# Performance work log

Hardware: AMD Instinct MI355X
Metric: run time of the kernel (lower is better)

## Reference

```python
import jax, jax.numpy as jnp
import numpy as np

NUM_HEADS = 8


def _mab(Q, K, Wq, bq, Wk, bk, Wv, bv, Wo, bo):
    # MAB with ln=False, dropout=0 (eval). Scale is sqrt(dim_V), matching source.
    B, Lq, _ = Q.shape
    Lk = K.shape[1]
    Dv = Wq.shape[1]
    dh = Dv // NUM_HEADS
    q = (Q @ Wq + bq).reshape(B, Lq, NUM_HEADS, dh).transpose(0, 2, 1, 3)
    k = (K @ Wk + bk).reshape(B, Lk, NUM_HEADS, dh).transpose(0, 2, 1, 3)
    v = (K @ Wv + bv).reshape(B, Lk, NUM_HEADS, dh).transpose(0, 2, 1, 3)
    A = jax.nn.softmax(jnp.einsum('bhqd,bhkd->bhqk', q, k) / jnp.sqrt(jnp.float32(Dv)), axis=-1)
    O = (q + jnp.einsum('bhqk,bhkd->bhqd', A, v)).transpose(0, 2, 1, 3).reshape(B, Lq, Dv)
    return O + jax.nn.relu(O @ Wo + bo)


def _forward(x, adj, gin_W, gin_b, geW1, geb1, geW2, geb2,
             gnW1, gnb1, gnW2, gnb2, goW, gob, S,
             mWq, mbq, mWk, mbk, mWv, mbv, mWo, mbo, finW, finb):
    B, V, T, D = x.shape
    Hd = gin_W.shape[1]
    # --- GNN encoder (adj path) ---
    h = x.reshape(B, V, T * D) @ gin_W + gin_b            # [B,V,H]
    # edge_mlp first linear on cat([h_i,h_j]) == h@Wi (row) + h@Wj (col); avoids 2H concat
    Wi, Wj = geW1[:Hd], geW1[Hd:]
    pre = (h @ Wi)[:, :, None, :] + (h @ Wj)[:, None, :, :] + geb1   # [B,V,V,H]
    e = jax.nn.relu(jax.nn.relu(pre) @ geW2 + geb2)       # [B,V,V,H]
    agg = jnp.einsum('bijh,bij->bih', e, adj)             # mask * sum over j, fused
    node = jax.nn.relu(jax.nn.relu(agg @ gnW1 + gnb1) @ gnW2 + gnb2)
    enc = node @ goW + gob                                # [B,V,H]
    # --- decoder: PMA + SAB + SAB + Linear ---
    o = _mab(jnp.broadcast_to(S, (B,) + S.shape[1:]), enc,
             mWq[0], mbq[0], mWk[0], mbk[0], mWv[0], mbv[0], mWo[0], mbo[0])
    o = _mab(o, o, mWq[1], mbq[1], mWk[1], mbk[1], mWv[1], mbv[1], mWo[1], mbo[1])
    o = _mab(o, o, mWq[2], mbq[2], mWk[2], mbk[2], mWv[2], mbv[2], mWo[2], mbo[2])
    out = o @ finW + finb                                 # [B,num_slots,T*OD]
    return out.reshape(B, S.shape[1], T, finW.shape[1] // T)


def setup_inputs() -> dict:
    key = jax.random.key(0)
    ks = jax.random.split(key, 16)
    B, V, T, D = 4, 256, 12, 4
    H, NS, OD = 256, 16, 32

    def w(k, shape, s=0.02):
        return s * jax.random.normal(k, shape, jnp.float32)

    return {
        'x': jax.random.normal(ks[0], (B, V, T, D), jnp.float32),
        'adj': (jax.random.uniform(ks[1], (B, V, V)) > 0.5).astype(jnp.float32),
        'gin_W': w(ks[2], (T * D, H)), 'gin_b': jnp.zeros((H,), jnp.float32),
        'geW1': w(ks[3], (2 * H, H)), 'geb1': jnp.zeros((H,), jnp.float32),
        'geW2': w(ks[4], (H, H)), 'geb2': jnp.zeros((H,), jnp.float32),
        'gnW1': w(ks[5], (H, H)), 'gnb1': jnp.zeros((H,), jnp.float32),
        'gnW2': w(ks[6], (H, H)), 'gnb2': jnp.zeros((H,), jnp.float32),
        'goW': w(ks[7], (H, H)), 'gob': jnp.zeros((H,), jnp.float32),
        'S': w(ks[8], (1, NS, H), 0.05),
        'mWq': w(ks[9], (3, H, H)), 'mbq': jnp.zeros((3, H), jnp.float32),
        'mWk': w(ks[10], (3, H, H)), 'mbk': jnp.zeros((3, H), jnp.float32),
        'mWv': w(ks[11], (3, H, H)), 'mbv': jnp.zeros((3, H), jnp.float32),
        'mWo': w(ks[12], (3, H, H)), 'mbo': jnp.zeros((3, H), jnp.float32),
        'finW': w(ks[13], (H, T * OD)), 'finb': jnp.zeros((T * OD,), jnp.float32),
    }


def reference(x, adj, gin_W, gin_b, geW1, geb1, geW2, geb2,
              gnW1, gnb1, gnW2, gnb2, goW, gob, S,
              mWq, mbq, mWk, mbk, mWv, mbv, mWo, mbo, finW, finb):
    return _forward(x, adj, gin_W, gin_b, geW1, geb1, geW2, geb2,
                    gnW1, gnb1, gnW2, gnb2, goW, gob, S,
                    mWq, mbq, mWk, mbk, mWv, mbv, mWo, mbo, finW, finb)
```

## Files before the change

kernel.cpp:

```cpp
#include <hip/hip_runtime.h>
#include <hip/hip_bf16.h>

typedef unsigned short u16;
typedef __bf16 bf8v __attribute__((ext_vector_type(8)));
typedef float f4v __attribute__((ext_vector_type(4)));

__device__ __forceinline__ float b2f(u16 v) {
  union { unsigned u; float f; } x; x.u = ((unsigned)v) << 16; return x.f;
}
__device__ __forceinline__ u16 f2b(float f) {
  union { float f; unsigned u; } x; x.f = f;
  unsigned r = (x.u + 0x7FFFu + ((x.u >> 16) & 1u)) >> 16;
  return (u16)r;
}
__device__ __forceinline__ unsigned pkbf(float a, float b) {
  union { __hip_bfloat162 h; unsigned u; } c;
  c.h = __float22bfloat162_rn(make_float2(a, b));
  return c.u;
}
__device__ __forceinline__ void up2(unsigned u, float& lo, float& hi) {
  union { unsigned x; float f; } a, b;
  a.x = u << 16; b.x = u & 0xffff0000u; lo = a.f; hi = b.f;
}

#define NFRAG 16
struct HeadArgs {
  const float* fsrc[NFRAG];
  u16* fdst[NFRAG];
  int fstride[NFRAG];
  int fbase[NFRAG + 1];
  int fragTiles, prepBid, q1Bid;
  const float *x, *ginW, *ginb, *geW1;
  float* hWiF;
  u16* hWjB;
  const float *mbk, *mbv, *mbq, *S, *mWq;
  float *bkv0, *bqkv1, *bqkv2;
  u16* q1b;
};

__global__ __launch_bounds__(256) void k_head(HeadArgs a) {
  __shared__ __align__(16) char sm[46080];
  const int bid = blockIdx.x, t = threadIdx.x;

  if (bid < 64) {
    u16* As = (u16*)sm;
    float* xs = (float*)(sm + 33792);
    const int lane = t & 63, wv = t >> 6;
    const int m0 = (bid >> 2) * 64, n0 = (bid & 3) * 128;
    for (int idx = t; idx < 64 * 48; idx += 256)
      xs[idx] = a.x[(size_t)(m0 + idx / 48) * 48 + idx % 48];
    __syncthreads();
    {
      float w48[48];
#pragma unroll
      for (int k = 0; k < 48; k++) w48[k] = a.ginW[(size_t)k * 256 + t];
      const float bias = a.ginb[t];
      for (int rg = 0; rg < 16; rg++) {
        float acc[4] = {bias, bias, bias, bias};
#pragma unroll
        for (int k = 0; k < 48; k++) {
          const float w = w48[k];
#pragma unroll
          for (int r = 0; r < 4; r++) acc[r] += xs[(rg * 4 + r) * 48 + k] * w;
        }
#pragma unroll
        for (int r = 0; r < 4; r++) As[(rg * 4 + r) * 264 + t] = f2b(acc[r]);
      }
    }
    __syncthreads();
    f4v acc[4][2];
// ... 48 lines not shown
  const int pb = bid - 64;
  if (pb < a.fragTiles) {
    u16* ld = (u16*)sm;
    int j = 0;
    while (j + 1 < NFRAG && a.fbase[j + 1] <= pb) j++;
    const int localT = pb - a.fbase[j];
    const float* src = a.fsrc[j];
    const int Ns = a.fstride[j];
    const int n0 = localT * 16;
    {
      const float* s = src + (size_t)t * Ns + n0;
      const float4 v0 = ((const float4*)s)[0], v1 = ((const float4*)s)[1];
      const float4 v2 = ((const float4*)s)[2], v3 = ((const float4*)s)[3];
      unsigned* row = (unsigned*)(ld + t * 20);
      row[0] = pkbf(v0.x, v0.y); row[1] = pkbf(v0.z, v0.w);
      row[2] = pkbf(v1.x, v1.y); row[3] = pkbf(v1.z, v1.w);
      row[4] = pkbf(v2.x, v2.y); row[5] = pkbf(v2.z, v2.w);
      row[6] = pkbf(v3.x, v3.y); row[7] = pkbf(v3.z, v3.w);
    }
    __syncthreads();
    u16* dst = a.fdst[j] + (size_t)localT * 4096;
#pragma unroll
    for (int s2 = 0; s2 < 2; s2++) {
      const int o = t * 2 + s2, kt = o >> 6, lane = o & 63;
      const int nlo = lane & 15, bk = kt * 32 + ((lane >> 4) << 3);
      union { u16 h[8]; uint4 q; } pk;
#pragma unroll
      for (int j2 = 0; j2 < 8; j2++) pk.h[j2] = ld[(bk + j2) * 20 + nlo];
      *(uint4*)(dst + (size_t)(kt * 64 + lane) * 8) = pk.q;
    }
    return;
  }
  if (bid == a.prepBid) {
    a.bkv0[t] = a.mbk[t]; a.bkv0[256 + t] = a.mbv[t];
    a.bqkv1[t] = a.mbq[256 + t]; a.bqkv1[256 + t] = a.mbk[256 + t]; a.bqkv1[512 + t] = a.mbv[256 + t];
    a.bqkv2[t] = a.mbq[512 + t]; a.bqkv2[256 + t] = a.mbk[512 + t]; a.bqkv2[512 + t] = a.mbv[512 + t];
    return;
  }
  if (bid == a.q1Bid) {
    float* Ss = (float*)sm;
    for (int idx = t; idx < 4096; idx += 256) Ss[idx] = a.S[idx];
    __syncthreads();
    float acc[16];
#pragma unroll
    for (int r = 0; r < 16; r++) acc[r] = 0.f;
    for (int k = 0; k < 256; k++) {
      const float w = a.mWq[(size_t)k * 256 + t];
#pragma unroll
      for (int r = 0; r < 16; r++) acc[r] += Ss[r * 256 + k] * w;
    }
    const float bq = a.mbq[t];
#pragma unroll
    for (int r = 0; r < 16; r++) a.q1b[r * 256 + t] = f2b(acc[r] + bq);
    return;
  }
}

__global__ __launch_bounds__(256) void k_edge(
    const float* __restrict__ hWiF, const u16* __restrict__ hWjB,
    const float* __restrict__ adj, const float* __restrict__ geb1,
    const u16* __restrict__ fragW2, const float* __restrict__ geb2,
    u16* __restrict__ aggB) {
  __shared__ __align__(16) u16 As[64 * 280];
  __shared__ float hi[256];
  __shared__ int jlist[256];
  __shared__ int cnt;
  const int t = threadIdx.x, lane = t & 63, wv = t >> 6;
  const int b = blockIdx.x >> 8, i = blockIdx.x & 255;
  if (t == 0) cnt = 0;
  __syncthreads();
  {
    const float a = adj[(size_t)(b * 256 + i) * 256 + t];
    hi[t] = hWiF[(size_t)(b * 256 + i) * 256 + t] + geb1[t];
    if (a != 0.f) { const int p = atomicAdd(&cnt, 1); jlist[p] = t; }
  }
  __syncthreads();
  const int nact = cnt;
  if (nact == 0) {
    if (lane < 16) {
#pragma unroll
      for (int nt = 0; nt < 4; nt++)
        aggB[(size_t)(b * 256 + i) * 256 + wv * 64 + nt * 16 + lane] = 0;
    }
    return;
  }
  const int nch = (nact + 63) >> 6;
  float bias2[4];
#pragma unroll
  for (int nt = 0; nt < 4; nt++) bias2[nt] = geb2[wv * 64 + nt * 16 + (lane & 15)];
  float aggAcc[4] = {0.f, 0.f, 0.f, 0.f};
  const u16* fw = fragW2 + lane * 8;
  const int r = t >> 2, q = t & 3;

  uint4 G[8];
  {
    const int rows0 = min(64, nact);
    const int j = (r < rows0) ? jlist[r] : jlist[0];
    const uint4* s4 = (const uint4*)(hWjB + (size_t)(b * 256 + j) * 256 + q * 64);
#pragma unroll
    for (int ii = 0; ii < 8; ii++) G[ii] = s4[ii];
  }

  for (int c = 0; c < nch; c++) {
    const int rows = min(64, nact - c * 64);
    {
      u16* dstrow = As + r * 280 + q * 72;
#pragma unroll
      for (int ii = 0; ii < 8; ii++) {
        const uint4 v = G[ii];
        const int k = q * 64 + ii * 8;
        float f0, f1, f2, f3, f4, f5, f6, f7;
        up2(v.x, f0, f1); up2(v.y, f2, f3); up2(v.z, f4, f5); up2(v.w, f6, f7);
        uint4 qd;
        qd.x = pkbf(fmaxf(f0 + hi[k + 0], 0.f), fmaxf(f1 + hi[k + 1], 0.f));
        qd.y = pkbf(fmaxf(f2 + hi[k + 2], 0.f), fmaxf(f3 + hi[k + 3], 0.f));
        qd.z = pkbf(fmaxf(f4 + hi[k + 4], 0.f), fmaxf(f5 + hi[k + 5], 0.f));
        qd.w = pkbf(fmaxf(f6 + hi[k + 6], 0.f), fmaxf(f7 + hi[k + 7], 0.f));
        *(uint4*)(dstrow + ii * 8) = qd;
      }
    }
    __syncthreads();
    if (c + 1 < nch) {
      const int rowsN = min(64, nact - (c + 1) * 64);
      const int j = (r < rowsN) ? jlist[(c + 1) * 64 + r] : jlist[0];
      const uint4* s4 = (const uint4*)(hWjB + (size_t)(b * 256 + j) * 256 + q * 64);
#pragma unroll
      for (int ii = 0; ii < 8; ii++) G[ii] = s4[ii];
    }
    f4v acc[4][4];
#pragma unroll
    for (int jt = 0; jt < 4; jt++)
#pragma unroll
      for (int nt = 0; nt < 4; nt++) acc[jt][nt] = (f4v){0.f, 0.f, 0.f, 0.f};
#pragma unroll
    for (int kt = 0; kt < 8; kt++) {
      bf8v af[4];
      const int coff = (kt >> 1) * 72 + (kt & 1) * 32 + ((lane >> 4) << 3);
#pragma unroll
      for (int jt = 0; jt < 4; jt++)
        af[jt] = *(const bf8v*)(As + (jt * 16 + (lane & 15)) * 280 + coff);
#pragma unroll
      for (int nt = 0; nt < 4; nt++) {
        const bf8v bw = *(const bf8v*)(fw + (size_t)((wv * 4 + nt) * 8 + kt) * 512);
#pragma unroll
        for (int jt = 0; jt < 4; jt++)
          acc[jt][nt] = __builtin_amdgcn_mfma_f32_16x16x32_bf16(af[jt], bw, acc[jt][nt], 0, 0, 0);
      }
    }
    const int rbase = (lane >> 4) * 4;
#pragma unroll
    for (int nt = 0; nt < 4; nt++) {
      float s = 0.f;
#pragma unroll
      for (int jt = 0; jt < 4; jt++) {
        const int r0 = jt * 16 + rbase;
#pragma unroll
        for (int rr = 0; rr < 4; rr++) {
          const float e = fmaxf(acc[jt][nt][rr] + bias2[nt], 0.f);
          s += (r0 + rr < rows) ? e : 0.f;
        }
      }
      s += __shfl_xor(s, 16);
      s += __shfl_xor(s, 32);
      aggAcc[nt] += s;
    }
    __syncthreads();
  }
  if (lane < 16) {
#pragma unroll
    for (int nt = 0; nt < 4; nt++) {
      const int n = wv * 64 + nt * 16 + lane;
      aggB[(size_t)(b * 256 + i) * 256 + n] = f2b(aggAcc[nt]);
    }
  }
}

#define NBLK 32

__device__ __forceinline__ void gridbar(int* cnt, int gen) {
  __syncthreads();
  if (threadIdx.x == 0) {
    __threadfence();
    __hip_atomic_fetch_add(cnt, 1, __ATOMIC_RELAXED, __HIP_MEMORY_SCOPE_AGENT);
    int it = 0;
    while (__hip_atomic_load(cnt, __ATOMIC_RELAXED, __HIP_MEMORY_SCOPE_AGENT) < NBLK * gen) {
      __builtin_amdgcn_s_sleep(8);
      if (((++it) & 255) == 0)
        __hip_atomic_fetch_add(cnt, 0, __ATOMIC_RELAXED, __HIP_MEMORY_SCOPE_AGENT);
    }
    __threadfence();
  }
  __syncthreads();
}

__device__ void g32(const u16* Al, const u16* frag, const float* bias, int relu,
                    u16* Ol, int t) {
  const int lane = t & 63, wv = t >> 6;
  f4v acc[2][4];
#pragma unroll
  for (int mt = 0; mt < 2; mt++)
#pragma unroll
    for (int nt = 0; nt < 4; nt++) acc[mt][nt] = (f4v){0.f, 0.f, 0.f, 0.f};
#pragma unroll
  for (int kt = 0; kt < 8; kt++) {
    bf8v af[2], bf[4];
#pragma unroll
    for (int mt = 0; mt < 2; mt++)
      af[mt] = *(const bf8v*)(Al + (mt * 16 + (lane & 15)) * 264 + kt * 32 + ((lane >> 4) << 3));
#pragma unroll
    for (int nt = 0; nt < 4; nt++)
      bf[nt] = *(const bf8v*)(frag + ((size_t)((wv * 4 + nt) * 8 + kt) * 64 + lane) * 8);
#pragma unroll
    for (int mt = 0; mt < 2; mt++)
#pragma unroll
      for (int nt = 0; nt < 4; nt++)
        acc[mt][nt] = __builtin_amdgcn_mfma_f32_16x16x32_bf16(af[mt], bf[nt], acc[mt][nt], 0, 0, 0);
  }
#pragma unroll
  for (int mt = 0; mt < 2; mt++)
#pragma unroll
    for (int nt = 0; nt < 4; nt++) {
      const int col = wv * 64 + nt * 16 + (lane & 15);
      const float bv = bias[col];
#pragma unroll
      for (int r = 0; r < 4; r++) {
        const int row = mt * 16 + ((lane >> 4) << 2) + r;
        float v = acc[mt][nt][r] + bv;
        if (relu) v = fmaxf(v, 0.f);
        Ol[row * 264 + col] = f2b(v);
      }
    }
}

__device__ void g32kv(const u16* Al, const u16* frag, const float* bias,
                      u16* outG, int t) {
  const int lane = t & 63, wv = t >> 6;
  f4v acc[2][8];
#pragma unroll
  for (int mt = 0; mt < 2; mt++)
#pragma unroll
    for (int nt = 0; nt < 8; nt++) acc[mt][nt] = (f4v){0.f, 0.f, 0.f, 0.f};
#pragma unroll
  for (int kt = 0; kt < 8; kt++) {
    bf8v af[2];
#pragma unroll
    for (int mt = 0; mt < 2; mt++)
      af[mt] = *(const bf8v*)(Al + (mt * 16 + (lane & 15)) * 264 + kt * 32 + ((lane >> 4) << 3));
#pragma unroll
    for (int nt = 0; nt < 8; nt++) {
      const bf8v bf = *(const bf8v*)(frag + ((size_t)((wv * 8 + nt) * 8 + kt) * 64 + lane) * 8);
#pragma unroll
      for (int mt = 0; mt < 2; mt++)
        acc[mt][nt] = __builtin_amdgcn_mfma_f32_16x16x32_bf16(af[mt], bf, acc[mt][nt], 0, 0, 0);
    }
  }
#pragma unroll
  for (int mt = 0; mt < 2; mt++)
#pragma unroll
    for (int nt = 0; nt < 8; nt++) {
      const int col = wv * 128 + nt * 16 + (lane & 15);
      const float bv = bias[col];
#pragma unroll
      for (int r = 0; r < 4; r++) {
        const int row = mt * 16 + ((lane >> 4) << 2) + r;
        outG[(size_t)row * 512 + col] = f2b(acc[mt][nt][r] + bv);
      }
    }
}

__device__ void attn_tile(const u16* __restrict__ qbuf,
                          const u16* __restrict__ kbuf, const u16* __restrict__ vbuf,
                          float* __restrict__ oF, u16* __restrict__ oB,
                          int b, int hd, float* qs, float* sc, float* vs, int t) {
  const int lane = t & 63, wv = t >> 6;
  const int Lk = 256;
  if (t < 64) {
    const int row = t >> 2, part = t & 3;
    const uint4 q4 = *(const uint4*)(qbuf + (size_t)row * 256 + hd * 32 + part * 8);
    float f0, f1, f2, f3, f4, f5, f6, f7;
    up2(q4.x, f0, f1); up2(q4.y, f2, f3); up2(q4.z, f4, f5); up2(q4.w, f6, f7);
    float4* d = (float4*)(qs + row * 32 + part * 8);
    d[0] = make_float4(f0, f1, f2, f3);
    d[1] = make_float4(f4, f5, f6, f7);
  }
  __syncthreads();
  {
    float kv[32];
    const uint4* kp = (const uint4*)(kbuf + (size_t)(b * Lk + t) * 512 + hd * 32);
#pragma unroll
    for (int c4 = 0; c4 < 4; c4++) {
      const uint4 k4 = kp[c4];
      up2(k4.x, kv[c4 * 8 + 0], kv[c4 * 8 + 1]);
      up2(k4.y, kv[c4 * 8 + 2], kv[c4 * 8 + 3]);
      up2(k4.z, kv[c4 * 8 + 4], kv[c4 * 8 + 5]);
      up2(k4.w, kv[c4 * 8 + 6], kv[c4 * 8 + 7]);
    }
    for (int r = 0; r < 16; r++) {
      float s = 0.f;
#pragma unroll
      for (int d = 0; d < 32; d++) s += qs[r * 32 + d] * kv[d];
      sc[r * 256 + t] = s * 0.0625f;
    }
  }
  __syncthreads();
  for (int r = wv * 4; r < wv * 4 + 4; r++) {
    float v[4];
    float mx = -1e30f;
#pragma unroll
    for (int q2 = 0; q2 < 4; q2++) {
      v[q2] = sc[r * 256 + lane + q2 * 64];
      mx = fmaxf(mx, v[q2]);
    }
    for (int off = 32; off; off >>= 1) mx = fmaxf(mx, __shfl_xor(mx, off));
    float sum = 0.f;
#pragma unroll
    for (int q2 = 0; q2 < 4; q2++) { v[q2] = __expf(v[q2] - mx); sum += v[q2]; }
    for (int off = 32; off; off >>= 1) sum += __shfl_xor(sum, off);
    const float inv = 1.f / sum;
#pragma unroll
    for (int q2 = 0; q2 < 4; q2++) sc[r * 256 + lane + q2 * 64] = v[q2] * inv;
  }
  __syncthreads();
  for (int u = t; u < 1024; u += 256) {
    const int row = u >> 2, part = u & 3;
    const uint4 v4 = *(const uint4*)(vbuf + (size_t)(b * Lk + row) * 512 + hd * 32 + part * 8);
    float f0, f1, f2, f3, f4, f5, f6, f7;
    up2(v4.x, f0, f1); up2(v4.y, f2, f3); up2(v4.z, f4, f5); up2(v4.w, f6, f7);
    float4* d = (float4*)(vs + row * 32 + part * 8);
    d[0] = make_float4(f0, f1, f2, f3);
    d[1] = make_float4(f4, f5, f6, f7);
  }
  __syncthreads();
  const int r0 = t >> 5, d = t & 31;
  float a0 = qs[r0 * 32 + d], a1 = qs[(r0 + 8) * 32 + d];
#pragma unroll 4
  for (int j = 0; j < Lk; j++) {
    const float vv = vs[j * 32 + d];
    a0 += sc[r0 * 256 + j] * vv;
    a1 += sc[(r0 + 8) * 256 + j] * vv;
  }
  const int c0 = hd * 32 + d;
  oF[(size_t)(b * 16 + r0) * 256 + c0] = a0;
  oB[(size_t)(b * 16 + r0) * 256 + c0] = f2b(a0);
  oF[(size_t)(b * 16 + r0 + 8) * 256 + c0] = a1;
  oB[(size_t)(b * 16 + r0 + 8) * 256 + c0] = f2b(a1);
}

__device__ void wprojG(const u16* __restrict__ o1b, const float* __restrict__ o1f,
                       const u16* __restrict__ frag, const float* __restrict__ bias,
                       u16* actL, float* residL, int b, int T, int lane) {
  f4v acc = (f4v){0.f, 0.f, 0.f, 0.f};
  const u16* abase = o1b + (size_t)(b * 16 + (lane & 15)) * 256 + ((lane >> 4) << 3);
  const u16* fbase = frag + ((size_t)(T * 8) * 64 + lane) * 8;
#pragma unroll
  for (int kt = 0; kt < 8; kt++)
    acc = __builtin_amdgcn_mfma_f32_16x16x32_bf16(*(const bf8v*)(abase + kt * 32),
                                                  *(const bf8v*)(fbase + (size_t)kt * 512), acc, 0, 0, 0);
  const int col = T * 16 + (lane & 15);
  const float bv = bias[col];
#pragma unroll
  for (int r = 0; r < 4; r++) {
    const int row = ((lane >> 4) << 2) + r;
    const float v = fmaxf(acc[r] + bv, 0.f) + o1f[(size_t)(b * 16 + row) * 256 + col];
    residL[row * 256 + col] = v;
    actL[row * 264 + col] = f2b(v);
  }
}

__device__ void wprojQ(const u16* actL, const u16* __restrict__ frag,
                       const float* __restrict__ bias, u16* qkvL, int T, int lane) {
  f4v acc = (f4v){0.f, 0.f, 0.f, 0.f};
  const u16* abase = actL + (lane & 15) * 264 + ((lane >> 4) << 3);
  const u16* fbase = frag + ((size_t)(T * 8) * 64 + lane) * 8;
#pragma unroll
  for (int kt = 0; kt < 8; kt++)
    acc = __builtin_amdgcn_mfma_f32_16x16x32_bf16(*(const bf8v*)(abase + kt * 32),
                                                  *(const bf8v*)(fbase + (size_t)kt * 512), acc, 0, 0, 0);
  const int col = T * 16 + (lane & 15);
// ... 79 lines not shown
  }
  float mx = fmaxf(fmaxf(p[0], p[1]), fmaxf(p[2], p[3]));
  mx = fmaxf(mx, __shfl_xor(mx, 16));
  mx = fmaxf(mx, __shfl_xor(mx, 32));
  float sum = 0.f;
#pragma unroll
  for (int c = 0; c < 4; c++) { p[c] = __expf(p[c] - mx); sum += p[c]; }
  sum += __shfl_xor(sum, 16);
  sum += __shfl_xor(sum, 32);
  const float inv = 1.f / sum;
#pragma unroll
  for (int c = 0; c < 4; c++) ps[r * 16 + cg * 4 + c] = p[c] * inv;
  float o[8];
#pragma unroll
  for (int j = 0; j < 8; j++) o[j] = qv[cg * 8 + j];
#pragma unroll
  for (int c = 0; c < 16; c++) {
    const float pv = ps[r * 16 + c];
    const uint4 v4 = *(const uint4*)(qkvL + c * 776 + 512 + hd * 32 + cg * 8);
    float v0, v1;
    up2(v4.x, v0, v1); o[0] += pv * v0; o[1] += pv * v1;
    up2(v4.y, v0, v1); o[2] += pv * v0; o[3] += pv * v1;
    up2(v4.z, v0, v1); o[4] += pv * v0; o[5] += pv * v1;
    up2(v4.w, v0, v1); o[6] += pv * v0; o[7] += pv * v1;
  }
  const int col0 = hd * 32 + cg * 8;
#pragma unroll
  for (int j = 0; j < 8; j++) residL[r * 256 + col0 + j] = o[j];
  unsigned* ob = (unsigned*)(actOut + r * 264 + col0);
  ob[0] = pkbf(o[0], o[1]); ob[1] = pkbf(o[2], o[3]);
  ob[2] = pkbf(o[4], o[5]); ob[3] = pkbf(o[6], o[7]);
}

struct TailArgs {
  const u16 *agg, *fGn1, *fGn2, *fGo, *fKV0, *fQKV1, *fQKV2, *fO0, *fO1, *fO2, *fFin, *q1b;
  const float *gnb1, *gnb2, *gob, *bkv0, *bqkv1, *bqkv2, *mbo, *finb;
  u16 *kv1, *o1b;
  float *o1f, *outF;
  int* bar;
};

__global__ __launch_bounds__(256) void k_tail(TailArgs a) {
  __shared__ __align__(16) char smem[62208];
  const int bid = blockIdx.x, t = threadIdx.x;
  const int lane = t & 63, w = t >> 6;

  {
    u16* actA = (u16*)smem;
    u16* actB = (u16*)(smem + 16896);
    const int r0 = bid * 32;
#pragma unroll
    for (int s = 0; s < 4; s++) {
      const int u = t * 4 + s, row = u >> 5, ch = u & 31;
      *(uint4*)(actA + row * 264 + ch * 8) =
          *(const uint4*)(a.agg + (size_t)(r0 + row) * 256 + ch * 8);
    }
    __syncthreads();
    g32(actA, a.fGn1, a.gnb1, 1, actB, t); __syncthreads();
    g32(actB, a.fGn2, a.gnb2, 1, actA, t); __syncthreads();
    g32(actA, a.fGo, a.gob, 0, actB, t); __syncthreads();
    g32kv(actB, a.fKV0, a.bkv0, a.kv1 + (size_t)r0 * 512, t);
  }
  gridbar(a.bar, 1);
  {
    float* qs = (float*)smem;
    float* sc = (float*)(smem + 2048);
    float* vs = (float*)(smem + 18432);
    attn_tile(a.q1b, a.kv1, a.kv1 + 256, a.o1f, a.o1b, bid >> 3, bid & 7, qs, sc, vs, t);
  }
  gridbar(a.bar, 2);
  if (bid >= 4) return;
  {
    const int b = bid;
    u16* act0 = (u16*)smem;
    u16* act1 = (u16*)(smem + 8448);
    u16* qkvL = (u16*)(smem + 16896);
    float* residL = (float*)(smem + 41728);
    float* psL = (float*)(smem + 58112);
    __syncthreads();
    for (int T = w; T < 16; T += 4) wprojG(a.o1b, a.o1f, a.fO0, a.mbo, act0, residL, b, T, lane);
    __syncthreads();
    for (int T = w; T < 48; T += 4) wprojQ(act0, a.fQKV1, a.bqkv1, qkvL, T, lane);
    __syncthreads();
    for (int hd = w; hd < 8; hd += 4) attnB(qkvL, residL, act1, psL + w * 256, hd, lane);
    __syncthreads();
    for (int T = w; T < 16; T += 4) wprojR(act1, a.fO1, a.mbo + 256, act0, residL, T, lane);
    __syncthreads();
    for (int T = w; T < 48; T += 4) wprojQ(act0, a.fQKV2, a.bqkv2, qkvL, T, lane);
    __syncthreads();
    for (int hd = w; hd < 8; hd += 4) attnB(qkvL, residL, act1, psL + w * 256, hd, lane);
    __syncthreads();
    for (int T = w; T < 16; T += 4) wprojR(act1, a.fO2, a.mbo + 512, act0, residL, T, lane);
    __syncthreads();
    for (int T = w; T < 24; T += 4)
      wprojF(act0, a.fFin, a.finb, a.outF + (size_t)b * 16 * 384, T, lane);
  }
}

extern "C" void kernel_launch(void* const* d_in, const int* in_sizes, int n_in,
                              void* d_out, int out_size, void* d_ws, size_t ws_size,
                              hipStream_t stream) {
  const float* x    = (const float*)d_in[0];
  const float* adj  = (const float*)d_in[1];
  const float* ginW = (const float*)d_in[2];
  const float* ginb = (const float*)d_in[3];
  const float* geW1 = (const float*)d_in[4];
  const float* geb1 = (const float*)d_in[5];
  const float* geW2 = (const float*)d_in[6];
  const float* geb2 = (const float*)d_in[7];
  const float* gnW1 = (const float*)d_in[8];
  const float* gnb1 = (const float*)d_in[9];
  const float* gnW2 = (const float*)d_in[10];
  const float* gnb2 = (const float*)d_in[11];
  const float* goW  = (const float*)d_in[12];
  const float* gob  = (const float*)d_in[13];
  const float* S    = (const float*)d_in[14];
  const float* mWq  = (const float*)d_in[15];
  const float* mbq  = (const float*)d_in[16];
  const float* mWk  = (const float*)d_in[17];
  const float* mbk  = (const float*)d_in[18];
  const float* mWv  = (const float*)d_in[19];
  const float* mbv  = (const float*)d_in[20];
  const float* mWo  = (const float*)d_in[21];
  const float* mbo  = (const float*)d_in[22];
  const float* finW = (const float*)d_in[23];
  const float* finb = (const float*)d_in[24];
  (void)in_sizes; (void)n_in; (void)out_size; (void)ws_size;

  char* wp = (char*)d_ws;
// ... 26 lines not shown
  u16* o1b      = (u16*)alloc(64 * 256 * 2);
  int* bar      = (int*)alloc(256);

  HeadArgs H{};
  int nj = 0, tiles = 0;
  auto addF = [&](const float* s, int stride, u16* d, int nT) {
    H.fsrc[nj] = s; H.fdst[nj] = d; H.fstride[nj] = stride; H.fbase[nj] = tiles;
    tiles += nT; nj++;
  };
  addF(geW2, 256, fW2, 16);
  addF(gnW1, 256, fGn1, 16);
  addF(gnW2, 256, fGn2, 16);
  addF(goW, 256, fGo, 16);
  addF(mWk, 256, fKV0, 16);
  addF(mWv, 256, fKV0 + 16 * 4096, 16);
  addF(mWq + 65536, 256, fQKV1, 16);
  addF(mWk + 65536, 256, fQKV1 + 16 * 4096, 16);
  addF(mWv + 65536, 256, fQKV1 + 32 * 4096, 16);
  addF(mWq + 131072, 256, fQKV2, 16);
  addF(mWk + 131072, 256, fQKV2 + 16 * 4096, 16);
  addF(mWv + 131072, 256, fQKV2 + 32 * 4096, 16);
  addF(mWo, 256, fO0, 16);
  addF(mWo + 65536, 256, fO1, 16);
  addF(mWo + 131072, 256, fO2, 16);
  addF(finW, 384, fFin, 24);
  H.fbase[nj] = tiles;
  H.fragTiles = tiles;
  H.prepBid = 64 + tiles;
  H.q1Bid = 64 + tiles + 1;
  H.x = x; H.ginW = ginW; H.ginb = ginb; H.geW1 = geW1;
  H.hWiF = hWiF; H.hWjB = hWjB;
  H.mbk = mbk; H.mbv = mbv; H.mbq = mbq; H.S = S; H.mWq = mWq;
  H.bkv0 = bkv0; H.bqkv1 = bqkv1; H.bqkv2 = bqkv2; H.q1b = q1b;

  TailArgs T{};
  T.agg = agg_b; T.fGn1 = fGn1; T.fGn2 = fGn2; T.fGo = fGo; T.fKV0 = fKV0;
  T.fQKV1 = fQKV1; T.fQKV2 = fQKV2; T.fO0 = fO0; T.fO1 = fO1; T.fO2 = fO2;
  T.fFin = fFin; T.q1b = q1b;
  T.gnb1 = gnb1; T.gnb2 = gnb2; T.gob = gob;
  T.bkv0 = bkv0; T.bqkv1 = bqkv1; T.bqkv2 = bqkv2; T.mbo = mbo; T.finb = finb;
  T.kv1 = kv1; T.o1b = o1b; T.o1f = o1f; T.outF = (float*)d_out;
  T.bar = bar;

  hipMemsetAsync(bar, 0, 256, stream);
  k_head<<<dim3(64 + tiles + 2), dim3(256), 0, stream>>>(H);
  k_edge<<<dim3(1024), dim3(256), 0, stream>>>(hWiF, hWjB, adj, geb1, fW2, geb2, agg_b);
  k_tail<<<dim3(NBLK), dim3(256), 0, stream>>>(T);
}
```

Baseline: 259.7 us.

## Fuse edge kernel with node MLP and attention via counter barrier; split tail

Merges the edge aggregation kernel with the node MLP, KV projection and PMA attention stages into one 1024-block kernel. All blocks increment a global counter and the first 32 blocks spin on it before continuing, replacing a kernel boundary and the memset with an in-kernel reset done in the head kernel. The final SAB stages move to a separate 4-block kernel, and the KV projection is split into halves to cut register use. It relies on the first 32 blocks making progress while the other blocks finish, and it adds spin-wait costs on those 32 blocks.

```diff
diff --git a/kernel.cpp b/kernel.cpp
--- a/kernel.cpp
+++ b/kernel.cpp
@@ -36,6 +36,7 @@
   const float *mbk, *mbv, *mbq, *S, *mWq;
   float *bkv0, *bqkv1, *bqkv2;
   u16* q1b;
+  int* bar;
 };
 
 __global__ __launch_bounds__(256) void k_head(HeadArgs a) {
@@ -150,6 +151,7 @@
     return;
   }
   if (bid == a.prepBid) {
+    if (t < 8) a.bar[t] = 0;
     a.bkv0[t] = a.mbk[t]; a.bkv0[256 + t] = a.mbv[t];
     a.bqkv1[t] = a.mbq[256 + t]; a.bqkv1[256 + t] = a.mbk[256 + t]; a.bqkv1[512 + t] = a.mbv[256 + t];
     a.bqkv2[t] = a.mbq[512 + t]; a.bqkv2[256 + t] = a.mbk[512 + t]; a.bqkv2[512 + t] = a.mbv[512 + t];
@@ -172,143 +174,6 @@
     for (int r = 0; r < 16; r++) a.q1b[r * 256 + t] = f2b(acc[r] + bq);
     return;
   }
-}
-
-__global__ __launch_bounds__(256) void k_edge(
-    const float* __restrict__ hWiF, const u16* __restrict__ hWjB,
-    const float* __restrict__ adj, const float* __restrict__ geb1,
-    const u16* __restrict__ fragW2, const float* __restrict__ geb2,
-    u16* __restrict__ aggB) {
-  __shared__ __align__(16) u16 As[64 * 280];
-  __shared__ float hi[256];
-  __shared__ int jlist[256];
-  __shared__ int cnt;
-  const int t = threadIdx.x, lane = t & 63, wv = t >> 6;
-  const int b = blockIdx.x >> 8, i = blockIdx.x & 255;
-  if (t == 0) cnt = 0;
-  __syncthreads();
-  {
-    const float a = adj[(size_t)(b * 256 + i) * 256 + t];
-    hi[t] = hWiF[(size_t)(b * 256 + i) * 256 + t] + geb1[t];
-    if (a != 0.f) { const int p = atomicAdd(&cnt, 1); jlist[p] = t; }
-  }
-  __syncthreads();
-  const int nact = cnt;
-  if (nact == 0) {
-    if (lane < 16) {
-#pragma unroll
-      for (int nt = 0; nt < 4; nt++)
-        aggB[(size_t)(b * 256 + i) * 256 + wv * 64 + nt * 16 + lane] = 0;
-    }
-    return;
-  }
-  const int nch = (nact + 63) >> 6;
-  float bias2[4];
-#pragma unroll
-  for (int nt = 0; nt < 4; nt++) bias2[nt] = geb2[wv * 64 + nt * 16 + (lane & 15)];
-  float aggAcc[4] = {0.f, 0.f, 0.f, 0.f};
-  const u16* fw = fragW2 + lane * 8;
-  const int r = t >> 2, q = t & 3;
-
-  uint4 G[8];
-  {
-    const int rows0 = min(64, nact);
-    const int j = (r < rows0) ? jlist[r] : jlist[0];
-    const uint4* s4 = (const uint4*)(hWjB + (size_t)(b * 256 + j) * 256 + q * 64);
-#pragma unroll
-    for (int ii = 0; ii < 8; ii++) G[ii] = s4[ii];
-  }
-
-  for (int c = 0; c < nch; c++) {
-    const int rows = min(64, nact - c * 64);
-    {
-      u16* dstrow = As + r * 280 + q * 72;
-#pragma unroll
-      for (int ii = 0; ii < 8; ii++) {
-        const uint4 v = G[ii];
-        const int k = q * 64 + ii * 8;
-        float f0, f1, f2, f3, f4, f5, f6, f7;
-        up2(v.x, f0, f1); up2(v.y, f2, f3); up2(v.z, f4, f5); up2(v.w, f6, f7);
-        uint4 qd;
-        qd.x = pkbf(fmaxf(f0 + hi[k + 0], 0.f), fmaxf(f1 + hi[k + 1], 0.f));
-        qd.y = pkbf(fmaxf(f2 + hi[k + 2], 0.f), fmaxf(f3 + hi[k + 3], 0.f));
-        qd.z = pkbf(fmaxf(f4 + hi[k + 4], 0.f), fmaxf(f5 + hi[k + 5], 0.f));
-        qd.w = pkbf(fmaxf(f6 + hi[k + 6], 0.f), fmaxf(f7 + hi[k + 7], 0.f));
-        *(uint4*)(dstrow + ii * 8) = qd;
-      }
-    }
-    __syncthreads();
-    if (c + 1 < nch) {
-      const int rowsN = min(64, nact - (c + 1) * 64);
-      const int j = (r < rowsN) ? jlist[(c + 1) * 64 + r] : jlist[0];
-      const uint4* s4 = (const uint4*)(hWjB + (size_t)(b * 256 + j) * 256 + q * 64);
-#pragma unroll
-      for (int ii = 0; ii < 8; ii++) G[ii] = s4[ii];
-    }
-    f4v acc[4][4];
-#pragma unroll
-    for (int jt = 0; jt < 4; jt++)
-#pragma unroll
-      for (int nt = 0; nt < 4; nt++) acc[jt][nt] = (f4v){0.f, 0.f, 0.f, 0.f};
-#pragma unroll
-    for (int kt = 0; kt < 8; kt++) {
-      bf8v af[4];
-      const int coff = (kt >> 1) * 72 + (kt & 1) * 32 + ((lane >> 4) << 3);
-#pragma unroll
-      for (int jt = 0; jt < 4; jt++)
-        af[jt] = *(const bf8v*)(As + (jt * 16 + (lane & 15)) * 280 + coff);
-#pragma unroll
-      for (int nt = 0; nt < 4; nt++) {
-        const bf8v bw = *(const bf8v*)(fw + (size_t)((wv * 4 + nt) * 8 + kt) * 512);
-#pragma unroll
-        for (int jt = 0; jt < 4; jt++)
-          acc[jt][nt] = __builtin_amdgcn_mfma_f32_16x16x32_bf16(af[jt], bw, acc[jt][nt], 0, 0, 0);
-      }
-    }
-    const int rbase = (lane >> 4) * 4;
-#pragma unroll
-    for (int nt = 0; nt < 4; nt++) {
-      float s = 0.f;
-#pragma unroll
-      for (int jt = 0; jt < 4; jt++) {
-        const int r0 = jt * 16 + rbase;
-#pragma unroll
-        for (int rr = 0; rr < 4; rr++) {
-          const float e = fmaxf(acc[jt][nt][rr] + bias2[nt], 0.f);
-          s += (r0 + rr < rows) ? e : 0.f;
-        }
-      }
-      s += __shfl_xor(s, 16);
-      s += __shfl_xor(s, 32);
-      aggAcc[nt] += s;
-    }
-    __syncthreads();
-  }
-  if (lane < 16) {
-#pragma unroll
-    for (int nt = 0; nt < 4; nt++) {
-      const int n = wv * 64 + nt * 16 + lane;
-      aggB[(size_t)(b * 256 + i) * 256 + n] = f2b(aggAcc[nt]);
-    }
-  }
-}
-
-#define NBLK 32
-
-__device__ __forceinline__ void gridbar(int* cnt, int gen) {
-  __syncthreads();
-  if (threadIdx.x == 0) {
-    __threadfence();
-    __hip_atomic_fetch_add(cnt, 1, __ATOMIC_RELAXED, __HIP_MEMORY_SCOPE_AGENT);
-    int it = 0;
-    while (__hip_atomic_load(cnt, __ATOMIC_RELAXED, __HIP_MEMORY_SCOPE_AGENT) < NBLK * gen) {
-      __builtin_amdgcn_s_sleep(8);
-      if (((++it) & 255) == 0)
-        __hip_atomic_fetch_add(cnt, 0, __ATOMIC_RELAXED, __HIP_MEMORY_SCOPE_AGENT);
-    }
-    __threadfence();
-  }
-  __syncthreads();
 }
 
 __device__ void g32(const u16* Al, const u16* frag, const float* bias, int relu,
@@ -350,14 +215,14 @@
     }
 }
 
-__device__ void g32kv(const u16* Al, const u16* frag, const float* bias,
-                      u16* outG, int t) {
+__device__ void g32kvh(const u16* Al, const u16* frag, const float* bias,
+                       u16* outG, int half, int t) {
   const int lane = t & 63, wv = t >> 6;
-  f4v acc[2][8];
+  f4v acc[2][4];
 #pragma unroll
   for (int mt = 0; mt < 2; mt++)
 #pragma unroll
-    for (int nt = 0; nt < 8; nt++) acc[mt][nt] = (f4v){0.f, 0.f, 0.f, 0.f};
+    for (int nt = 0; nt < 4; nt++) acc[mt][nt] = (f4v){0.f, 0.f, 0.f, 0.f};
 #pragma unroll
   for (int kt = 0; kt < 8; kt++) {
     bf8v af[2];
@@ -365,8 +230,9 @@
     for (int mt = 0; mt < 2; mt++)
       af[mt] = *(const bf8v*)(Al + (mt * 16 + (lane & 15)) * 264 + kt * 32 + ((lane >> 4) << 3));
 #pragma unroll
-    for (int nt = 0; nt < 8; nt++) {
-      const bf8v bf = *(const bf8v*)(frag + ((size_t)((wv * 8 + nt) * 8 + kt) * 64 + lane) * 8);
+    for (int nt = 0; nt < 4; nt++) {
+      const int T = half * 16 + wv * 4 + nt;
+      const bf8v bf = *(const bf8v*)(frag + ((size_t)(T * 8 + kt) * 64 + lane) * 8);
 #pragma unroll
       for (int mt = 0; mt < 2; mt++)
         acc[mt][nt] = __builtin_amdgcn_mfma_f32_16x16x32_bf16(af[mt], bf, acc[mt][nt], 0, 0, 0);
@@ -375,8 +241,8 @@
 #pragma unroll
   for (int mt = 0; mt < 2; mt++)
 #pragma unroll
-    for (int nt = 0; nt < 8; nt++) {
-      const int col = wv * 128 + nt * 16 + (lane & 15);
+    for (int nt = 0; nt < 4; nt++) {
+      const int col = half * 256 + wv * 64 + nt * 16 + (lane & 15);
       const float bv = bias[col];
 #pragma unroll
       for (int r = 0; r < 4; r++) {
@@ -386,82 +252,253 @@
     }
 }
 
-__device__ void attn_tile(const u16* __restrict__ qbuf,
-                          const u16* __restrict__ kbuf, const u16* __restrict__ vbuf,
-                          float* __restrict__ oF, u16* __restrict__ oB,
-                          int b, int hd, float* qs, float* sc, float* vs, int t) {
-  const int lane = t & 63, wv = t >> 6;
-  const int Lk = 256;
-  if (t < 64) {
-    const int row = t >> 2, part = t & 3;
-    const uint4 q4 = *(const uint4*)(qbuf + (size_t)row * 256 + hd * 32 + part * 8);
-    float f0, f1, f2, f3, f4, f5, f6, f7;
-    up2(q4.x, f0, f1); up2(q4.y, f2, f3); up2(q4.z, f4, f5); up2(q4.w, f6, f7);
-    float4* d = (float4*)(qs + row * 32 + part * 8);
-    d[0] = make_float4(f0, f1, f2, f3);
-    d[1] = make_float4(f4, f5, f6, f7);
-  }
-  __syncthreads();
+struct MidArgs {
+  const float *hWiF, *adj, *geb1, *geb2;
+  const u16 *hWjB, *fragW2;
+  u16* aggB;
+  const u16 *fGn1, *fGn2, *fGo, *fKV0, *q1b;
+  const float *gnb1, *gnb2, *gob, *bkv0;
+  u16 *kv1, *o1b;
+  float* o1f;
+  int* bar;
+};
+
+__global__ __launch_bounds__(256) void k_mid(MidArgs a) {
+  __shared__ __align__(16) char smem[38400];
+  const int t = threadIdx.x, lane = t & 63, wv = t >> 6;
+  const int bid = blockIdx.x;
+
   {
-    float kv[32];
-    const uint4* kp = (const uint4*)(kbuf + (size_t)(b * Lk + t) * 512 + hd * 32);
-#pragma unroll
-    for (int c4 = 0; c4 < 4; c4++) {
-      const uint4 k4 = kp[c4];
-      up2(k4.x, kv[c4 * 8 + 0], kv[c4 * 8 + 1]);
-      up2(k4.y, kv[c4 * 8 + 2], kv[c4 * 8 + 3]);
-      up2(k4.z, kv[c4 * 8 + 4], kv[c4 * 8 + 5]);
-      up2(k4.w, kv[c4 * 8 + 6], kv[c4 * 8 + 7]);
-    }
-    for (int r = 0; r < 16; r++) {
-      float s = 0.f;
-#pragma unroll
-      for (int d = 0; d < 32; d++) s += qs[r * 32 + d] * kv[d];
-      sc[r * 256 + t] = s * 0.0625f;
-    }
-  }
-  __syncthreads();
-  for (int r = wv * 4; r < wv * 4 + 4; r++) {
-    float v[4];
-    float mx = -1e30f;
-#pragma unroll
-    for (int q2 = 0; q2 < 4; q2++) {
-      v[q2] = sc[r * 256 + lane + q2 * 64];
-      mx = fmaxf(mx, v[q2]);
-    }
-    for (int off = 32; off; off >>= 1) mx = fmaxf(mx, __shfl_xor(mx, off));
-    float sum = 0.f;
-#pragma unroll
-    for (int q2 = 0; q2 < 4; q2++) { v[q2] = __expf(v[q2] - mx); sum += v[q2]; }
-    for (int off = 32; off; off >>= 1) sum += __shfl_xor(sum, off);
-    const float inv = 1.f / sum;
-#pragma unroll
-    for (int q2 = 0; q2 < 4; q2++) sc[r * 256 + lane + q2 * 64] = v[q2] * inv;
-  }
-  __syncthreads();
-  for (int u = t; u < 1024; u += 256) {
-    const int row = u >> 2, part = u & 3;
-    const uint4 v4 = *(const uint4*)(vbuf + (size_t)(b * Lk + row) * 512 + hd * 32 + part * 8);
-    float f0, f1, f2, f3, f4, f5, f6, f7;
-    up2(v4.x, f0, f1); up2(v4.y, f2, f3); up2(v4.z, f4, f5); up2(v4.w, f6, f7);
-    float4* d = (float4*)(vs + row * 32 + part * 8);
-    d[0] = make_float4(f0, f1, f2, f3);
-    d[1] = make_float4(f4, f5, f6, f7);
-  }
-  __syncthreads();
-  const int r0 = t >> 5, d = t & 31;
-  float a0 = qs[r0 * 32 + d], a1 = qs[(r0 + 8) * 32 + d];
+    u16* As = (u16*)smem;
+    float* hi = (float*)(smem + 35840);
+    int* jlist = (int*)(smem + 36864);
+    int* cntp = (int*)(smem + 37888);
+    const int b = bid >> 8, i = bid & 255;
+    if (t == 0) *cntp = 0;
+    __syncthreads();
+    {
+      const float av = a.adj[(size_t)(b * 256 + i) * 256 + t];
+      hi[t] = a.hWiF[(size_t)(b * 256 + i) * 256 + t] + a.geb1[t];
+      if (av != 0.f) { const int p = atomicAdd(cntp, 1); jlist[p] = t; }
+    }
+    __syncthreads();
+    const int nact = *cntp;
+    if (nact == 0) {
+      if (lane < 16) {
+#pragma unroll
+        for (int nt = 0; nt < 4; nt++)
+          a.aggB[(size_t)(b * 256 + i) * 256 + wv * 64 + nt * 16 + lane] = 0;
+      }
+    } else {
+      const int nch = (nact + 63) >> 6;
+      float bias2[4];
+#pragma unroll
+      for (int nt = 0; nt < 4; nt++) bias2[nt] = a.geb2[wv * 64 + nt * 16 + (lane & 15)];
+      float aggAcc[4] = {0.f, 0.f, 0.f, 0.f};
+      const u16* fw = a.fragW2 + lane * 8;
+      const int r = t >> 2, q = t & 3;
+      uint4 G[8];
+      {
+        const int rows0 = min(64, nact);
+        const int j = (r < rows0) ? jlist[r] : jlist[0];
+        const uint4* s4 = (const uint4*)(a.hWjB + (size_t)(b * 256 + j) * 256 + q * 64);
+#pragma unroll
+        for (int ii = 0; ii < 8; ii++) G[ii] = s4[ii];
+      }
+      for (int c = 0; c < nch; c++) {
+        const int rows = min(64, nact - c * 64);
+        {
+          u16* dstrow = As + r * 280 + q * 72;
+#pragma unroll
+          for (int ii = 0; ii < 8; ii++) {
+            const uint4 v = G[ii];
+            const int k = q * 64 + ii * 8;
+            float f0, f1, f2, f3, f4, f5, f6, f7;
+            up2(v.x, f0, f1); up2(v.y, f2, f3); up2(v.z, f4, f5); up2(v.w, f6, f7);
+            uint4 qd;
+            qd.x = pkbf(fmaxf(f0 + hi[k + 0], 0.f), fmaxf(f1 + hi[k + 1], 0.f));
+            qd.y = pkbf(fmaxf(f2 + hi[k + 2], 0.f), fmaxf(f3 + hi[k + 3], 0.f));
+            qd.z = pkbf(fmaxf(f4 + hi[k + 4], 0.f), fmaxf(f5 + hi[k + 5], 0.f));
+            qd.w = pkbf(fmaxf(f6 + hi[k + 6], 0.f), fmaxf(f7 + hi[k + 7], 0.f));
+            *(uint4*)(dstrow + ii * 8) = qd;
+          }
+        }
+        __syncthreads();
+        if (c + 1 < nch) {
+          const int rowsN = min(64, nact - (c + 1) * 64);
+          const int j = (r < rowsN) ? jlist[(c + 1) * 64 + r] : jlist[0];
+          const uint4* s4 = (const uint4*)(a.hWjB + (size_t)(b * 256 + j) * 256 + q * 64);
+#pragma unroll
+          for (int ii = 0; ii < 8; ii++) G[ii] = s4[ii];
+        }
+        f4v acc[4][4];
+#pragma unroll
+        for (int jt = 0; jt < 4; jt++)
+#pragma unroll
+          for (int nt = 0; nt < 4; nt++) acc[jt][nt] = (f4v){0.f, 0.f, 0.f, 0.f};
+#pragma unroll
+        for (int kt = 0; kt < 8; kt++) {
+          bf8v af[4];
+          const int coff = (kt >> 1) * 72 + (kt & 1) * 32 + ((lane >> 4) << 3);
+#pragma unroll
+          for (int jt = 0; jt < 4; jt++)
+            af[jt] = *(const bf8v*)(As + (jt * 16 + (lane & 15)) * 280 + coff);
+#pragma unroll
+          for (int nt = 0; nt < 4; nt++) {
+            const bf8v bw = *(const bf8v*)(fw + (size_t)((wv * 4 + nt) * 8 + kt) * 512);
+#pragma unroll
+            for (int jt = 0; jt < 4; jt++)
+              acc[jt][nt] = __builtin_amdgcn_mfma_f32_16x16x32_bf16(af[jt], bw, acc[jt][nt], 0, 0, 0);
+          }
+        }
+        const int rbase = (lane >> 4) * 4;
+#pragma unroll
+        for (int nt = 0; nt < 4; nt++) {
+          float s = 0.f;
+#pragma unroll
+          for (int jt = 0; jt < 4; jt++) {
+            const int r0 = jt * 16 + rbase;
+#pragma unroll
+            for (int rr = 0; rr < 4; rr++) {
+              const float e = fmaxf(acc[jt][nt][rr] + bias2[nt], 0.f);
+              s += (r0 + rr < rows) ? e : 0.f;
+            }
+          }
+          s += __shfl_xor(s, 16);
+          s += __shfl_xor(s, 32);
+          aggAcc[nt] += s;
+        }
+        __syncthreads();
+      }
+      if (lane < 16) {
+#pragma unroll
+        for (int nt = 0; nt < 4; nt++) {
+          const int n = wv * 64 + nt * 16 + lane;
+          a.aggB[(size_t)(b * 256 + i) * 256 + n] = f2b(aggAcc[nt]);
+        }
+      }
+    }
+  }
+  __syncthreads();
+  if (t == 0) {
+    __threadfence();
+    __hip_atomic_fetch_add(a.bar + 0, 1, __ATOMIC_RELAXED, __HIP_MEMORY_SCOPE_AGENT);
+  }
+  if (bid >= 32) return;
+  if (t == 0) {
+    int it = 0;
+    while (__hip_atomic_load(a.bar + 0, __ATOMIC_RELAXED, __HIP_MEMORY_SCOPE_AGENT) < 1024) {
+      __builtin_amdgcn_s_sleep(8);
+      if (((++it) & 255) == 0)
+        __hip_atomic_fetch_add(a.bar + 0, 0, __ATOMIC_RELAXED, __HIP_MEMORY_SCOPE_AGENT);
+    }
+    __threadfence();
+  }
+  __syncthreads();
+
+  {
+    u16* actA = (u16*)smem;
+    u16* actB = (u16*)(smem + 16896);
+    const int r0 = bid * 32;
+#pragma unroll
+    for (int s = 0; s < 4; s++) {
+      const int u = t * 4 + s, row = u >> 5, ch = u & 31;
+      *(uint4*)(actA + row * 264 + ch * 8) =
+          *(const uint4*)(a.aggB + (size_t)(r0 + row) * 256 + ch * 8);
+    }
+    __syncthreads();
+    g32(actA, a.fGn1, a.gnb1, 1, actB, t); __syncthreads();
+    g32(actB, a.fGn2, a.gnb2, 1, actA, t); __syncthreads();
+    g32(actA, a.fGo, a.gob, 0, actB, t); __syncthreads();
+    g32kvh(actB, a.fKV0, a.bkv0, a.kv1 + (size_t)r0 * 512, 0, t);
+    g32kvh(actB, a.fKV0, a.bkv0, a.kv1 + (size_t)r0 * 512, 1, t);
+  }
+  __syncthreads();
+  if (t == 0) {
+    __threadfence();
+    __hip_atomic_fetch_add(a.bar + 1, 1, __ATOMIC_RELAXED, __HIP_MEMORY_SCOPE_AGENT);
+    int it = 0;
+    while (__hip_atomic_load(a.bar + 1, __ATOMIC_RELAXED, __HIP_MEMORY_SCOPE_AGENT) < 32) {
+      __builtin_amdgcn_s_sleep(8);
+      if (((++it) & 255) == 0)
+        __hip_atomic_fetch_add(a.bar + 1, 0, __ATOMIC_RELAXED, __HIP_MEMORY_SCOPE_AGENT);
+    }
+    __threadfence();
+  }
+  __syncthreads();
+
+  {
+    float* qs = (float*)smem;
+    float* sc = (float*)(smem + 2048);
+    u16* vsB = (u16*)(smem + 18432);
+    const int b = bid >> 3, hd = bid & 7;
+    const int Lk = 256;
+    if (t < 64) {
+      const int row = t >> 2, part = t & 3;
+      const uint4 q4 = *(const uint4*)(a.q1b + (size_t)row * 256 + hd * 32 + part * 8);
+      float f0, f1, f2, f3, f4, f5, f6, f7;
+      up2(q4.x, f0, f1); up2(q4.y, f2, f3); up2(q4.z, f4, f5); up2(q4.w, f6, f7);
+      float4* d = (float4*)(qs + row * 32 + part * 8);
+      d[0] = make_float4(f0, f1, f2, f3);
+      d[1] = make_float4(f4, f5, f6, f7);
+    }
+    for (int idx = t; idx < 1024; idx += 256) {
+      const int row = idx >> 2, part = idx & 3;
+      *(uint4*)(vsB + row * 32 + part * 8) =
+          *(const uint4*)(a.kv1 + (size_t)(b * 256 + row) * 512 + 256 + hd * 32 + part * 8);
+    }
+    __syncthreads();
+    {
+      float kv[32];
+      const uint4* kp = (const uint4*)(a.kv1 + (size_t)(b * Lk + t) * 512 + hd * 32);
+#pragma unroll
+      for (int c4 = 0; c4 < 4; c4++) {
+        const uint4 k4 = kp[c4];
+        up2(k4.x, kv[c4 * 8 + 0], kv[c4 * 8 + 1]);
+        up2(k4.y, kv[c4 * 8 + 2], kv[c4 * 8 + 3]);
+        up2(k4.z, kv[c4 * 8 + 4], kv[c4 * 8 + 5]);
+        up2(k4.w, kv[c4 * 8 + 6], kv[c4 * 8 + 7]);
+      }
+      for (int r = 0; r < 16; r++) {
+        float s = 0.f;
+#pragma unroll
+        for (int d = 0; d < 32; d++) s += qs[r * 32 + d] * kv[d];
+        sc[r * 256 + t] = s * 0.0625f;
+      }
+    }
+    __syncthreads();
+    for (int r = wv * 4; r < wv * 4 + 4; r++) {
+      float v[4];
+      float mx = -1e30f;
+#pragma unroll
+      for (int q2 = 0; q2 < 4; q2++) {
+        v[q2] = sc[r * 256 + lane + q2 * 64];
+        mx = fmaxf(mx, v[q2]);
+      }
+      for (int off = 32; off; off >>= 1) mx = fmaxf(mx, __shfl_xor(mx, off));
+      float sum = 0.f;
+#pragma unroll
+      for (int q2 = 0; q2 < 4; q2++) { v[q2] = __expf(v[q2] - mx); sum += v[q2]; }
+      for (int off = 32; off; off >>= 1) sum += __shfl_xor(sum, off);
+      const float inv = 1.f / sum;
+#pragma unroll
+      for (int q2 = 0; q2 < 4; q2++) sc[r * 256 + lane + q2 * 64] = v[q2] * inv;
+    }
+    __syncthreads();
+    const int r0 = t >> 5, d = t & 31;
+    float a0 = qs[r0 * 32 + d], a1 = qs[(r0 + 8) * 32 + d];
 #pragma unroll 4
-  for (int j = 0; j < Lk; j++) {
-    const float vv = vs[j * 32 + d];
-    a0 += sc[r0 * 256 + j] * vv;
-    a1 += sc[(r0 + 8) * 256 + j] * vv;
-  }
-  const int c0 = hd * 32 + d;
-  oF[(size_t)(b * 16 + r0) * 256 + c0] = a0;
-  oB[(size_t)(b * 16 + r0) * 256 + c0] = f2b(a0);
-  oF[(size_t)(b * 16 + r0 + 8) * 256 + c0] = a1;
-  oB[(size_t)(b * 16 + r0 + 8) * 256 + c0] = f2b(a1);
+    for (int j = 0; j < Lk; j++) {
+      const float vv = b2f(vsB[j * 32 + d]);
+      a0 += sc[r0 * 256 + j] * vv;
+      a1 += sc[(r0 + 8) * 256 + j] * vv;
+    }
+    const int c0 = hd * 32 + d;
+    a.o1f[(size_t)(b * 16 + r0) * 256 + c0] = a0;
+    a.o1b[(size_t)(b * 16 + r0) * 256 + c0] = f2b(a0);
+    a.o1f[(size_t)(b * 16 + r0 + 8) * 256 + c0] = a1;
+    a.o1b[(size_t)(b * 16 + r0 + 8) * 256 + c0] = f2b(a1);
+  }
 }
 
 __device__ void wprojG(const u16* __restrict__ o1b, const float* __restrict__ o1f,
@@ -607,69 +644,40 @@
   ob[2] = pkbf(o[4], o[5]); ob[3] = pkbf(o[6], o[7]);
 }
 
-struct TailArgs {
-  const u16 *agg, *fGn1, *fGn2, *fGo, *fKV0, *fQKV1, *fQKV2, *fO0, *fO1, *fO2, *fFin, *q1b;
-  const float *gnb1, *gnb2, *gob, *bkv0, *bqkv1, *bqkv2, *mbo, *finb;
-  u16 *kv1, *o1b;
-  float *o1f, *outF;
-  int* bar;
+struct Tail3Args {
+  const u16 *fQKV1, *fQKV2, *fO0, *fO1, *fO2, *fFin;
+  const float *bqkv1, *bqkv2, *mbo, *finb;
+  const u16* o1b;
+  const float* o1f;
+  float* outF;
 };
 
-__global__ __launch_bounds__(256) void k_tail(TailArgs a) {
+__global__ __launch_bounds__(256) void k_tail3(Tail3Args a) {
   __shared__ __align__(16) char smem[62208];
-  const int bid = blockIdx.x, t = threadIdx.x;
+  const int b = blockIdx.x, t = threadIdx.x;
   const int lane = t & 63, w = t >> 6;
-
-  {
-    u16* actA = (u16*)smem;
-    u16* actB = (u16*)(smem + 16896);
-    const int r0 = bid * 32;
-#pragma unroll
-    for (int s = 0; s < 4; s++) {
-      const int u = t * 4 + s, row = u >> 5, ch = u & 31;
-      *(uint4*)(actA + row * 264 + ch * 8) =
-          *(const uint4*)(a.agg + (size_t)(r0 + row) * 256 + ch * 8);
-    }
-    __syncthreads();
-    g32(actA, a.fGn1, a.gnb1, 1, actB, t); __syncthreads();
-    g32(actB, a.fGn2, a.gnb2, 1, actA, t); __syncthreads();
-    g32(actA, a.fGo, a.gob, 0, actB, t); __syncthreads();
-    g32kv(actB, a.fKV0, a.bkv0, a.kv1 + (size_t)r0 * 512, t);
-  }
-  gridbar(a.bar, 1);
-  {
-    float* qs = (float*)smem;
-    float* sc = (float*)(smem + 2048);
-    float* vs = (float*)(smem + 18432);
-    attn_tile(a.q1b, a.kv1, a.kv1 + 256, a.o1f, a.o1b, bid >> 3, bid & 7, qs, sc, vs, t);
-  }
-  gridbar(a.bar, 2);
-  if (bid >= 4) return;
-  {
-    const int b = bid;
-    u16* act0 = (u16*)smem;
-    u16* act1 = (u16*)(smem + 8448);
-    u16* qkvL = (u16*)(smem + 16896);
-    float* residL = (float*)(smem + 41728);
-    float* psL = (float*)(smem + 58112);
-    __syncthreads();
-    for (int T = w; T < 16; T += 4) wprojG(a.o1b, a.o1f, a.fO0, a.mbo, act0, residL, b, T, lane);
-    __syncthreads();
-    for (int T = w; T < 48; T += 4) wprojQ(act0, a.fQKV1, a.bqkv1, qkvL, T, lane);
-    __syncthreads();
-    for (int hd = w; hd < 8; hd += 4) attnB(qkvL, residL, act1, psL + w * 256, hd, lane);
-    __syncthreads();
-    for (int T = w; T < 16; T += 4) wprojR(act1, a.fO1, a.mbo + 256, act0, residL, T, lane);
-    __syncthreads();
-    for (int T = w; T < 48; T += 4) wprojQ(act0, a.fQKV2, a.bqkv2, qkvL, T, lane);
-    __syncthreads();
-    for (int hd = w; hd < 8; hd += 4) attnB(qkvL, residL, act1, psL + w * 256, hd, lane);
-    __syncthreads();
-    for (int T = w; T < 16; T += 4) wprojR(act1, a.fO2, a.mbo + 512, act0, residL, T, lane);
-    __syncthreads();
-    for (int T = w; T < 24; T += 4)
-      wprojF(act0, a.fFin, a.finb, a.outF + (size_t)b * 16 * 384, T, lane);
-  }
+  u16* act0 = (u16*)smem;
+  u16* act1 = (u16*)(smem + 8448);
+  u16* qkvL = (u16*)(smem + 16896);
+  float* residL = (float*)(smem + 41728);
+  float* psL = (float*)(smem + 58112);
+
+  for (int T = w; T < 16; T += 4) wprojG(a.o1b, a.o1f, a.fO0, a.mbo, act0, residL, b, T, lane);
+  __syncthreads();
+  for (int T = w; T < 48; T += 4) wprojQ(act0, a.fQKV1, a.bqkv1, qkvL, T, lane);
+  __syncthreads();
+  for (int hd = w; hd < 8; hd += 4) attnB(qkvL, residL, act1, psL + w * 256, hd, lane);
+  __syncthreads();
+  for (int T = w; T < 16; T += 4) wprojR(act1, a.fO1, a.mbo + 256, act0, residL, T, lane);
+  __syncthreads();
+  for (int T = w; T < 48; T += 4) wprojQ(act0, a.fQKV2, a.bqkv2, qkvL, T, lane);
+  __syncthreads();
+  for (int hd = w; hd < 8; hd += 4) attnB(qkvL, residL, act1, psL + w * 256, hd, lane);
+  __syncthreads();
+  for (int T = w; T < 16; T += 4) wprojR(act1, a.fO2, a.mbo + 512, act0, residL, T, lane);
+  __syncthreads();
+  for (int T = w; T < 24; T += 4)
+    wprojF(act0, a.fFin, a.finb, a.outF + (size_t)b * 16 * 384, T, lane);
 }
 
 extern "C" void kernel_launch(void* const* d_in, const int* in_sizes, int n_in,
@@ -762,18 +770,21 @@
   H.hWiF = hWiF; H.hWjB = hWjB;
   H.mbk = mbk; H.mbv = mbv; H.mbq = mbq; H.S = S; H.mWq = mWq;
   H.bkv0 = bkv0; H.bqkv1 = bqkv1; H.bqkv2 = bqkv2; H.q1b = q1b;
-
-  TailArgs T{};
-  T.agg = agg_b; T.fGn1 = fGn1; T.fGn2 = fGn2; T.fGo = fGo; T.fKV0 = fKV0;
-  T.fQKV1 = fQKV1; T.fQKV2 = fQKV2; T.fO0 = fO0; T.fO1 = fO1; T.fO2 = fO2;
-  T.fFin = fFin; T.q1b = q1b;
-  T.gnb1 = gnb1; T.gnb2 = gnb2; T.gob = gob;
-  T.bkv0 = bkv0; T.bqkv1 = bqkv1; T.bqkv2 = bqkv2; T.mbo = mbo; T.finb = finb;
-  T.kv1 = kv1; T.o1b = o1b; T.o1f = o1f; T.outF = (float*)d_out;
-  T.bar = bar;
-
-  hipMemsetAsync(bar, 0, 256, stream);
+  H.bar = bar;
+
+  MidArgs M{};
+  M.hWiF = hWiF; M.adj = adj; M.geb1 = geb1; M.geb2 = geb2;
+  M.hWjB = hWjB; M.fragW2 = fW2; M.aggB = agg_b;
+  M.fGn1 = fGn1; M.fGn2 = fGn2; M.fGo = fGo; M.fKV0 = fKV0; M.q1b = q1b;
+  M.gnb1 = gnb1; M.gnb2 = gnb2; M.gob = gob; M.bkv0 = bkv0;
+  M.kv1 = kv1; M.o1b = o1b; M.o1f = o1f; M.bar = bar;
+
+  Tail3Args T3{};
+  T3.fQKV1 = fQKV1; T3.fQKV2 = fQKV2; T3.fO0 = fO0; T3.fO1 = fO1; T3.fO2 = fO2;
+  T3.fFin = fFin; T3.bqkv1 = bqkv1; T3.bqkv2 = bqkv2; T3.mbo = mbo; T3.finb = finb;
+  T3.o1b = o1b; T3.o1f = o1f; T3.outF = (float*)d_out;
+
   k_head<<<dim3(64 + tiles + 2), dim3(256), 0, stream>>>(H);
-  k_edge<<<dim3(1024), dim3(256), 0, stream>>>(hWiF, hWjB, adj, geb1, fW2, geb2, agg_b);
-  k_tail<<<dim3(NBLK), dim3(256), 0, stream>>>(T);
-}
+  k_mid<<<dim3(1024), dim3(256), 0, stream>>>(M);
+  k_tail3<<<dim3(4), dim3(256), 0, stream>>>(T3);
+}
```

Result: slower. 306.5 us (+18.0%).
